# Optimization experiments

Measured on AMD Instinct MI355X. Metric: run time of the kernel, lower is better.

## Reference

```python
import jax, jax.numpy as jnp
import numpy as np

N_NODES = 50000
N_EDGES = 800000
IN_FEAT = 128
OUT_FEAT = 128


def _glorot(key, shape):
    fan_in, fan_out = shape[1], shape[0]
    lim = jnp.sqrt(6.0 / (fan_in + fan_out))
    return jax.random.uniform(key, shape, jnp.float32, -lim, lim)


def setup_inputs() -> dict:
    key = jax.random.key(0)
    ks = jax.random.split(key, 9)
    x = jax.random.normal(ks[0], (N_NODES, IN_FEAT), jnp.float32)
    edge_index = jax.random.randint(ks[1], (2, N_EDGES), 0, N_NODES, jnp.int64)
    # SAGEConv params: lin_l applied to aggregated neighbors (with bias),
    # lin_r applied to root features (no bias) -- PyG default mean aggregation.
    W1l = _glorot(ks[2], (OUT_FEAT, IN_FEAT)); b1l = jnp.zeros((OUT_FEAT,), jnp.float32)
    W1r = _glorot(ks[3], (OUT_FEAT, IN_FEAT))
    W2l = _glorot(ks[4], (OUT_FEAT, OUT_FEAT)); b2l = jnp.zeros((OUT_FEAT,), jnp.float32)
    W2r = _glorot(ks[5], (OUT_FEAT, OUT_FEAT))
    Wlin = _glorot(ks[6], (2, OUT_FEAT)); blin = jnp.zeros((2,), jnp.float32)
    return {"x": x, "edge_index": edge_index,
            "W1l": W1l, "b1l": b1l, "W1r": W1r,
            "W2l": W2l, "b2l": b2l, "W2r": W2r,
            "Wlin": Wlin, "blin": blin}


def _sage_conv(x, src, dst, Wl, bl, Wr, n_nodes):
    # mean-aggregate neighbor features at destination nodes
    agg_sum = jax.ops.segment_sum(x[src], dst, num_segments=n_nodes)  # [N, F]
    deg = jax.ops.segment_sum(jnp.ones((src.shape[0],), x.dtype), dst, num_segments=n_nodes)
    agg = agg_sum / jnp.maximum(deg, 1.0)[:, None]
    return agg @ Wl.T + bl + x @ Wr.T


def reference(x, edge_index, W1l, b1l, W1r, W2l, b2l, W2r, Wlin, blin):
    src, dst = edge_index[0], edge_index[1]
    n = x.shape[0]
    h = _sage_conv(x, src, dst, W1l, b1l, W1r, n)
    h = jax.nn.relu(h)  # dropout is identity in eval mode
    h = _sage_conv(h, src, dst, W2l, b2l, W2r, n)
    h = jax.nn.relu(h)
    logits = h @ Wlin.T + blin  # [N, 2]
    return jax.nn.log_softmax(logits, axis=1)
```

## Files before the change

### kernel.cpp

```cpp
#include <hip/hip_runtime.h>
#include <math.h>

#define N_NODES 50000
#define N_EDGES 800000
#define F 128
#define ELL_CAP 64
#define NBUCK 196
#define BIN_CAP 97
#define BUCK_CAP 4608
#define EDGE_BLKS 125
#define EPR (N_EDGES / EDGE_BLKS)
#define CVT_BLKS 6250

typedef __attribute__((ext_vector_type(8))) short short8;
typedef __attribute__((ext_vector_type(4))) float float4v;

__device__ inline unsigned short f2bf(float f) {
    unsigned int u = __builtin_bit_cast(unsigned int, f);
    u += 0x7FFF + ((u >> 16) & 1);
    return (unsigned short)(u >> 16);
}
__device__ inline float bf2f_lo(unsigned int u) {
    return __builtin_bit_cast(float, u << 16);
}
__device__ inline float bf2f_hi(unsigned int u) {
    return __builtin_bit_cast(float, u & 0xFFFF0000u);
}
__device__ inline float i8f(unsigned int u, int k) {
    return (float)((signed char)(u >> (k * 8)));
}

__global__ __launch_bounds__(256) void prep1(const float* __restrict__ x,
                                             const int* __restrict__ src,
                                             const int* __restrict__ dst,
                                             const float* __restrict__ W1l,
                                             const float* __restrict__ W1r,
                                             const float* __restrict__ W2l,
                                             const float* __restrict__ W2r,
                                             unsigned short* __restrict__ xb,
                                             unsigned char* __restrict__ xq,
                                             float* __restrict__ xscale,
                                             int* __restrict__ tails,
                                             unsigned int* __restrict__ bucketEdges,
                                             unsigned short* __restrict__ P1,
                                             unsigned short* __restrict__ P2) {
    int blk = blockIdx.x;
    int tid = threadIdx.x;
    if (blk < EDGE_BLKS) {
        __shared__ int bin_cnt[NBUCK];
        __shared__ unsigned int bins[NBUCK * BIN_CAP];
        for (int i = tid; i < NBUCK; i += 256) bin_cnt[i] = 0;
        __syncthreads();
        int base = blk * EPR;
        for (int i = tid; i < EPR; i += 256) {
            int d = dst[base + i];
            int s = src[base + i];
            int lb = d >> 8;
            int pos = atomicAdd(&bin_cnt[lb], 1);
            if (pos < BIN_CAP)
                bins[lb * BIN_CAP + pos] = ((unsigned int)(d & 255) << 16) | (unsigned int)s;
        }
        __syncthreads();
        if (tid < NBUCK) {
            int c = bin_cnt[tid]; if (c > BIN_CAP) c = BIN_CAP;
            int rb = atomicAdd(&tails[tid], c);
            unsigned int* dp = bucketEdges + (size_t)tid * BUCK_CAP;
            for (int i = 0; i < c; ++i) {
                int p = rb + i;
                if (p < BUCK_CAP) dp[p] = bins[tid * BIN_CAP + i];
            }
        }
    } else if (blk < EDGE_BLKS + CVT_BLKS) {
        int row = (blk - EDGE_BLKS) * 8 + (tid >> 5);
        int hl = tid & 31;
        float4 v = ((const float4*)x)[row * 32 + hl];
        float m = fmaxf(fmaxf(fabsf(v.x), fabsf(v.y)), fmaxf(fabsf(v.z), fabsf(v.w)));
        #pragma unroll
        for (int off = 1; off < 32; off <<= 1) m = fmaxf(m, __shfl_xor(m, off));
        float inv = m > 0.f ? 127.f / m : 0.f;
        int q0 = (int)rintf(v.x * inv), q1 = (int)rintf(v.y * inv);
        int q2 = (int)rintf(v.z * inv), q3 = (int)rintf(v.w * inv);
        unsigned int qp = (q0 & 255) | ((q1 & 255) << 8) | ((q2 & 255) << 16) | ((q3 & 255) << 24);
        ((unsigned int*)xq)[row * 32 + hl] = qp;
        unsigned int p0 = (unsigned int)f2bf(v.x) | ((unsigned int)f2bf(v.y) << 16);
        unsigned int p1 = (unsigned int)f2bf(v.z) | ((unsigned int)f2bf(v.w) << 16);
        ((uint2*)xb)[row * 32 + hl] = make_uint2(p0, p1);
        if (hl == 0) xscale[row] = m * (1.f / 127.f);
    } else {
        int pblk = blk - (EDGE_BLKS + CVT_BLKS);
        int t = (pblk & 15) * 256 + tid;
        int lane = t & 63;
        int ct = (t >> 6) & 7;
        int ks = t >> 9;
        const float* Wl = (pblk < 16) ? W1l : W2l;
        const float* Wr = (pblk < 16) ? W1r : W2r;
        unsigned short* P = (pblk < 16) ? P1 : P2;
        int col = ct * 16 + (lane & 15);
        int kbase = (ks & 3) * 32 + (lane >> 4) * 8;
        const float* W = (ks < 4) ? Wl : Wr;
        unsigned short* dp = P + (size_t)t * 8;
        #pragma unroll
        for (int j = 0; j < 8; ++j) dp[j] = f2bf(W[col * F + kbase + j]);
    }
}

__global__ __launch_bounds__(256) void ell_build(const int* __restrict__ tails,
                                                 const unsigned int* __restrict__ bucketEdges,
                                                 int* __restrict__ cnt,
                                                 unsigned short* __restrict__ nbr) {
    __shared__ int cl[256];
    __shared__ unsigned short ell[256 * ELL_CAP];
    int b = blockIdx.x;
    int tid = threadIdx.x;
    cl[tid] = 0;
    __syncthreads();
    int T = tails[b]; if (T > BUCK_CAP) T = BUCK_CAP;
    const unsigned int* eb = bucketEdges + (size_t)b * BUCK_CAP;
    for (int i = tid; i < T; i += 256) {
        unsigned int rec = eb[i];
        int nib = rec >> 16;
        int pos = atomicAdd(&cl[nib], 1);
        if (pos < ELL_CAP) ell[nib * ELL_CAP + pos] = (unsigned short)(rec & 0xFFFFu);
    }
    __syncthreads();
    int nb0 = b * 256;
    int nn = N_NODES - nb0; if (nn > 256) nn = 256;
    if (tid < nn) cnt[nb0 + tid] = cl[tid];
    const uint4* s4 = (const uint4*)ell;
    uint4* d4 = (uint4*)(nbr + (size_t)nb0 * ELL_CAP);
    int n4 = nn * (ELL_CAP * 2 / 16);
    for (int i = tid; i < n4; i += 256) d4[i] = s4[i];
}

__global__ __launch_bounds__(256) void aggregate_q(const unsigned char* __restrict__ Xq,
                                                   const float* __restrict__ xs,
                                                   const int* __restrict__ cnt,
                                                   const unsigned short* __restrict__ nbr,
                                                   unsigned short* __restrict__ agg) {
    int tid = threadIdx.x;
    int wave = tid >> 6;
    int lane = tid & 63;
    int half = lane >> 5;
    int hl = lane & 31;
    int node = blockIdx.x * 8 + wave * 2 + half;

    int degt = cnt[node];
    int deg = degt < ELL_CAP ? degt : ELL_CAP;
    const unsigned short* nb = nbr + node * ELL_CAP;
    const unsigned int* Xu = (const unsigned int*)Xq;

    float a0 = 0.f, a1 = 0.f, a2 = 0.f, a3 = 0.f;
    int s = 0;
    for (; s + 4 <= deg; s += 4) {
        ushort4 nv = *(const ushort4*)(nb + s);
        unsigned int g0 = Xu[nv.x * 32 + hl]; float s0 = xs[nv.x];
        unsigned int g1 = Xu[nv.y * 32 + hl]; float s1 = xs[nv.y];
        unsigned int g2 = Xu[nv.z * 32 + hl]; float s2 = xs[nv.z];
        unsigned int g3 = Xu[nv.w * 32 + hl]; float s3 = xs[nv.w];
        a0 += i8f(g0, 0) * s0 + i8f(g1, 0) * s1 + i8f(g2, 0) * s2 + i8f(g3, 0) * s3;
        a1 += i8f(g0, 1) * s0 + i8f(g1, 1) * s1 + i8f(g2, 1) * s2 + i8f(g3, 1) * s3;
        a2 += i8f(g0, 2) * s0 + i8f(g1, 2) * s1 + i8f(g2, 2) * s2 + i8f(g3, 2) * s3;
        a3 += i8f(g0, 3) * s0 + i8f(g1, 3) * s1 + i8f(g2, 3) * s2 + i8f(g3, 3) * s3;
    }
    for (; s < deg; ++s) {
        int v = nb[s];
        unsigned int g = Xu[v * 32 + hl]; float sc = xs[v];
        a0 += i8f(g, 0) * sc; a1 += i8f(g, 1) * sc;
        a2 += i8f(g, 2) * sc; a3 += i8f(g, 3) * sc;
    }
    float inv = 1.0f / (float)(degt > 0 ? degt : 1);
    unsigned int p0 = (unsigned int)f2bf(a0 * inv) | ((unsigned int)f2bf(a1 * inv) << 16);
    unsigned int p1 = (unsigned int)f2bf(a2 * inv) | ((unsigned int)f2bf(a3 * inv) << 16);
    *(uint2*)(agg + (size_t)node * F + hl * 4) = make_uint2(p0, p1);
}

__global__ __launch_bounds__(256) void sage_gemm(const unsigned short* __restrict__ Abf,
                                                 const unsigned short* __restrict__ Bbf,
                                                 const unsigned short* __restrict__ Pw,
                                                 const float* __restrict__ bias,
                                                 unsigned short* __restrict__ Hout,
                                                 unsigned char* __restrict__ Hq,
                                                 float* __restrict__ Hscale,
                                                 const float* __restrict__ Wlin,
                                                 const float* __restrict__ blin,
                                                 float* __restrict__ out, int mode) {
    int lane = threadIdx.x & 63;
    int wave = threadIdx.x >> 6;
    int r0 = blockIdx.x * 64 + wave * 16;
    int rowA = r0 + (lane & 15);
    if (rowA >= N_NODES) rowA = N_NODES - 1;
    int kg = lane >> 4;

    short8 af[4], bfr[4];
    const short8* Ap = (const short8*)(Abf + (size_t)rowA * F);
    const short8* Bp = (const short8*)(Bbf + (size_t)rowA * F);
    #pragma unroll
    for (int ks = 0; ks < 4; ++ks) {
        af[ks]  = Ap[ks * 4 + kg];
        bfr[ks] = Bp[ks * 4 + kg];
    }

    const short8* Wp = (const short8*)Pw;
    float4v acc[8];
    #pragma unroll
    for (int ct = 0; ct < 8; ++ct) {
        float4v c = {0.f, 0.f, 0.f, 0.f};
        #pragma unroll
        for (int ks = 0; ks < 4; ++ks)
            c = __builtin_amdgcn_mfma_f32_16x16x32_bf16(af[ks], Wp[(ks * 8 + ct) * 64 + lane], c, 0, 0, 0);
        #pragma unroll
        for (int ks = 0; ks < 4; ++ks)
            c = __builtin_amdgcn_mfma_f32_16x16x32_bf16(bfr[ks], Wp[((ks + 4) * 8 + ct) * 64 + lane], c, 0, 0, 0);
        acc[ct] = c;
    }

    int colb = lane & 15;
    int rq = lane >> 4;
    #pragma unroll
    for (int ct = 0; ct < 8; ++ct) {
        float bv = bias[ct * 16 + colb];
        #pragma unroll
        for (int i = 0; i < 4; ++i)
            acc[ct][i] = fmaxf(acc[ct][i] + bv, 0.f);
    }

    if (mode == 0) {
        #pragma unroll
        for (int ct = 0; ct < 8; ++ct) {
            #pragma unroll
            for (int i = 0; i < 4; ++i) {
                int row = r0 + rq * 4 + i;
                if (row < N_NODES)
                    Hout[(size_t)row * F + ct * 16 + colb] = f2bf(acc[ct][i]);
            }
        }
        #pragma unroll
        for (int i = 0; i < 4; ++i) {
            float m = 0.f;
            #pragma unroll
            for (int ct = 0; ct < 8; ++ct) m = fmaxf(m, acc[ct][i]);
            #pragma unroll
            for (int off = 1; off < 16; off <<= 1) m = fmaxf(m, __shfl_xor(m, off));
            float inv = m > 0.f ? 127.f / m : 0.f;
            int row = r0 + rq * 4 + i;
            if (row < N_NODES) {
                if (colb == 0) Hscale[row] = m * (1.f / 127.f);
                #pragma unroll
                for (int ct = 0; ct < 8; ++ct) {
                    int q = (int)rintf(acc[ct][i] * inv);
                    Hq[(size_t)row * F + ct * 16 + colb] = (unsigned char)q;
                }
            }
        }
    } else {
        float w0[8], w1[8];
        #pragma unroll
        for (int ct = 0; ct < 8; ++ct) {
            w0[ct] = Wlin[ct * 16 + colb];
            w1[ct] = Wlin[F + ct * 16 + colb];
        }
        #pragma unroll
        for (int i = 0; i < 4; ++i) {
            float p0 = 0.f, p1 = 0.f;
            #pragma unroll
            for (int ct = 0; ct < 8; ++ct) {
                p0 += acc[ct][i] * w0[ct];
                p1 += acc[ct][i] * w1[ct];
            }
            #pragma unroll
            for (int off = 1; off < 16; off <<= 1) {
                p0 += __shfl_xor(p0, off);
                p1 += __shfl_xor(p1, off);
            }
            int row = r0 + rq * 4 + i;
            if (colb == 0 && row < N_NODES) {
                float a = p0 + blin[0];
                float b = p1 + blin[1];
                float m = fmaxf(a, b);
                float lse = m + logf(expf(a - m) + expf(b - m));
                out[(size_t)row * 2 + 0] = a - lse;
                out[(size_t)row * 2 + 1] = b - lse;
            }
        }
    }
}

extern "C" void kernel_launch(void* const* d_in, const int* in_sizes, int n_in,
                              void* d_out, int out_size, void* d_ws, size_t ws_size,
                              hipStream_t stream) {
    const float* x    = (const float*)d_in[0];
    const int*   ei   = (const int*)d_in[1];
    const float* W1l  = (const float*)d_in[2];
    const float* b1l  = (const float*)d_in[3];
    const float* W1r  = (const float*)d_in[4];
    const float* W2l  = (const float*)d_in[5];
    const float* b2l  = (const float*)d_in[6];
    const float* W2r  = (const float*)d_in[7];
    const float* Wlin = (const float*)d_in[8];
    const float* blin = (const float*)d_in[9];
    float* out = (float*)d_out;

    const int* src = ei;
    const int* dst = ei + N_EDGES;

    char* ws = (char*)d_ws;
    int*            tails  = (int*)ws;
    unsigned int*   bEdge  = (unsigned int*)(ws + 4096);
    int*            cnt    = (int*)(ws + 3620864);
    unsigned short* nbr    = (unsigned short*)(ws + 3821568);
    unsigned short* xb     = (unsigned short*)(ws + 10221568);
    unsigned short* h1b    = (unsigned short*)(ws + 23021568);
    unsigned short* aggb   = (unsigned short*)(ws + 35821568);
    unsigned short* P1     = (unsigned short*)(ws + 48621568);
    unsigned short* P2     = (unsigned short*)(ws + 48687104);
    unsigned char*  xq     = (unsigned char*)(ws + 48752640);
    unsigned char*  h1q    = (unsigned char*)(ws + 55152640);
    float*          xscale = (float*)(ws + 61552640);
    float*          h1scale= (float*)(ws + 61752640);

    hipMemsetAsync(tails, 0, NBUCK * sizeof(int), stream);

    prep1<<<EDGE_BLKS + CVT_BLKS + 32, 256, 0, stream>>>(x, src, dst, W1l, W1r, W2l, W2r,
                                                         xb, xq, xscale, tails, bEdge, P1, P2);
    ell_build<<<NBUCK, 256, 0, stream>>>(tails, bEdge, cnt, nbr);

    aggregate_q<<<6250, 256, 0, stream>>>(xq, xscale, cnt, nbr, aggb);
    sage_gemm<<<782, 256, 0, stream>>>(aggb, xb, P1, b1l, h1b, h1q, h1scale,
                                       nullptr, nullptr, nullptr, 0);

    aggregate_q<<<6250, 256, 0, stream>>>(h1q, h1scale, cnt, nbr, aggb);
    sage_gemm<<<782, 256, 0, stream>>>(aggb, h1b, P2, b2l, nullptr, nullptr, nullptr,
                                       Wlin, blin, out, 1);
}
```

Before: 122.1 us.

## Fuse neighbor aggregation into SAGE GEMM via LDS and drop bf16 copies

Merges the aggregation kernel into the GEMM kernel. Each 64-row block gathers int8 neighbor features into a padded LDS tile as bf16, then runs the MFMA GEMM reading A from LDS. The bf16 copies of x and h1 are removed, and the root operand is dequantized from int8 on the fly. This cuts two launches and the global round trip of the aggregate and bf16 feature buffers. In exchange, each block now has fewer waves doing the gather (782 blocks instead of 6250), which may reduce latency hiding, and the root term loses precision from int8 input.

```diff
diff --git a/kernel.cpp b/kernel.cpp
--- a/kernel.cpp
+++ b/kernel.cpp
@@ -11,6 +11,7 @@
 #define EDGE_BLKS 125
 #define EPR (N_EDGES / EDGE_BLKS)
 #define CVT_BLKS 6250
+#define LROW 136
 
 typedef __attribute__((ext_vector_type(8))) short short8;
 typedef __attribute__((ext_vector_type(4))) float float4v;
@@ -20,14 +21,16 @@
     u += 0x7FFF + ((u >> 16) & 1);
     return (unsigned short)(u >> 16);
 }
-__device__ inline float bf2f_lo(unsigned int u) {
-    return __builtin_bit_cast(float, u << 16);
-}
-__device__ inline float bf2f_hi(unsigned int u) {
-    return __builtin_bit_cast(float, u & 0xFFFF0000u);
-}
 __device__ inline float i8f(unsigned int u, int k) {
     return (float)((signed char)(u >> (k * 8)));
+}
+__device__ inline short8 deq8(uint2 g, float sc) {
+    short8 r;
+    #pragma unroll
+    for (int j = 0; j < 4; ++j) r[j] = (short)f2bf(i8f(g.x, j) * sc);
+    #pragma unroll
+    for (int j = 0; j < 4; ++j) r[4 + j] = (short)f2bf(i8f(g.y, j) * sc);
+    return r;
 }
 
 __global__ __launch_bounds__(256) void prep1(const float* __restrict__ x,
@@ -37,7 +40,6 @@
                                              const float* __restrict__ W1r,
                                              const float* __restrict__ W2l,
                                              const float* __restrict__ W2r,
-                                             unsigned short* __restrict__ xb,
                                              unsigned char* __restrict__ xq,
                                              float* __restrict__ xscale,
                                              int* __restrict__ tails,
@@ -82,9 +84,6 @@
         int q2 = (int)rintf(v.z * inv), q3 = (int)rintf(v.w * inv);
         unsigned int qp = (q0 & 255) | ((q1 & 255) << 8) | ((q2 & 255) << 16) | ((q3 & 255) << 24);
         ((unsigned int*)xq)[row * 32 + hl] = qp;
-        unsigned int p0 = (unsigned int)f2bf(v.x) | ((unsigned int)f2bf(v.y) << 16);
-        unsigned int p1 = (unsigned int)f2bf(v.z) | ((unsigned int)f2bf(v.w) << 16);
-        ((uint2*)xb)[row * 32 + hl] = make_uint2(p0, p1);
         if (hl == 0) xscale[row] = m * (1.f / 127.f);
     } else {
         int pblk = blk - (EDGE_BLKS + CVT_BLKS);
@@ -132,72 +131,82 @@
     for (int i = tid; i < n4; i += 256) d4[i] = s4[i];
 }
 
-__global__ __launch_bounds__(256) void aggregate_q(const unsigned char* __restrict__ Xq,
-                                                   const float* __restrict__ xs,
-                                                   const int* __restrict__ cnt,
-                                                   const unsigned short* __restrict__ nbr,
-                                                   unsigned short* __restrict__ agg) {
+__global__ __launch_bounds__(256) void sage_fused(const unsigned char* __restrict__ Xq,
+                                                  const float* __restrict__ xs,
+                                                  const int* __restrict__ cnt,
+                                                  const unsigned short* __restrict__ nbr,
+                                                  const unsigned short* __restrict__ Pw,
+                                                  const float* __restrict__ bias,
+                                                  unsigned char* __restrict__ Hq,
+                                                  float* __restrict__ Hscale,
+                                                  const float* __restrict__ Wlin,
+                                                  const float* __restrict__ blin,
+                                                  float* __restrict__ out, int mode) {
+    __shared__ unsigned short sA[64 * LROW];
     int tid = threadIdx.x;
     int wave = tid >> 6;
     int lane = tid & 63;
-    int half = lane >> 5;
-    int hl = lane & 31;
-    int node = blockIdx.x * 8 + wave * 2 + half;
-
-    int degt = cnt[node];
-    int deg = degt < ELL_CAP ? degt : ELL_CAP;
-    const unsigned short* nb = nbr + node * ELL_CAP;
-    const unsigned int* Xu = (const unsigned int*)Xq;
-
-    float a0 = 0.f, a1 = 0.f, a2 = 0.f, a3 = 0.f;
-    int s = 0;
-    for (; s + 4 <= deg; s += 4) {
-        ushort4 nv = *(const ushort4*)(nb + s);
-        unsigned int g0 = Xu[nv.x * 32 + hl]; float s0 = xs[nv.x];
-        unsigned int g1 = Xu[nv.y * 32 + hl]; float s1 = xs[nv.y];
-        unsigned int g2 = Xu[nv.z * 32 + hl]; float s2 = xs[nv.z];
-        unsigned int g3 = Xu[nv.w * 32 + hl]; float s3 = xs[nv.w];
-        a0 += i8f(g0, 0) * s0 + i8f(g1, 0) * s1 + i8f(g2, 0) * s2 + i8f(g3, 0) * s3;
-        a1 += i8f(g0, 1) * s0 + i8f(g1, 1) * s1 + i8f(g2, 1) * s2 + i8f(g3, 1) * s3;
-        a2 += i8f(g0, 2) * s0 + i8f(g1, 2) * s1 + i8f(g2, 2) * s2 + i8f(g3, 2) * s3;
-        a3 += i8f(g0, 3) * s0 + i8f(g1, 3) * s1 + i8f(g2, 3) * s2 + i8f(g3, 3) * s3;
-    }
-    for (; s < deg; ++s) {
-        int v = nb[s];
-        unsigned int g = Xu[v * 32 + hl]; float sc = xs[v];
-        a0 += i8f(g, 0) * sc; a1 += i8f(g, 1) * sc;
-        a2 += i8f(g, 2) * sc; a3 += i8f(g, 3) * sc;
-    }
-    float inv = 1.0f / (float)(degt > 0 ? degt : 1);
-    unsigned int p0 = (unsigned int)f2bf(a0 * inv) | ((unsigned int)f2bf(a1 * inv) << 16);
-    unsigned int p1 = (unsigned int)f2bf(a2 * inv) | ((unsigned int)f2bf(a3 * inv) << 16);
-    *(uint2*)(agg + (size_t)node * F + hl * 4) = make_uint2(p0, p1);
-}
-
-__global__ __launch_bounds__(256) void sage_gemm(const unsigned short* __restrict__ Abf,
-                                                 const unsigned short* __restrict__ Bbf,
-                                                 const unsigned short* __restrict__ Pw,
-                                                 const float* __restrict__ bias,
-                                                 unsigned short* __restrict__ Hout,
-                                                 unsigned char* __restrict__ Hq,
-                                                 float* __restrict__ Hscale,
-                                                 const float* __restrict__ Wlin,
-                                                 const float* __restrict__ blin,
-                                                 float* __restrict__ out, int mode) {
-    int lane = threadIdx.x & 63;
-    int wave = threadIdx.x >> 6;
-    int r0 = blockIdx.x * 64 + wave * 16;
-    int rowA = r0 + (lane & 15);
-    if (rowA >= N_NODES) rowA = N_NODES - 1;
+    int nb0 = blockIdx.x * 64;
+
+    int q = lane >> 4;
+    int ql = lane & 15;
+    const uint2* Xu2 = (const uint2*)Xq;
+    #pragma unroll
+    for (int round = 0; round < 4; ++round) {
+        int r = wave * 16 + round * 4 + q;
+        int node = nb0 + r;
+        float a0 = 0.f, a1 = 0.f, a2 = 0.f, a3 = 0.f, a4 = 0.f, a5 = 0.f, a6 = 0.f, a7 = 0.f;
+        int degt = 0;
+        if (node < N_NODES) {
+            degt = cnt[node];
+            int deg = degt < ELL_CAP ? degt : ELL_CAP;
+            const unsigned short* nb = nbr + node * ELL_CAP;
+            int s = 0;
+            for (; s + 4 <= deg; s += 4) {
+                ushort4 nv = *(const ushort4*)(nb + s);
+                uint2 g0 = Xu2[nv.x * 16 + ql]; float s0 = xs[nv.x];
+                uint2 g1 = Xu2[nv.y * 16 + ql]; float s1 = xs[nv.y];
+                uint2 g2 = Xu2[nv.z * 16 + ql]; float s2 = xs[nv.z];
+                uint2 g3 = Xu2[nv.w * 16 + ql]; float s3 = xs[nv.w];
+                a0 += i8f(g0.x, 0) * s0 + i8f(g1.x, 0) * s1 + i8f(g2.x, 0) * s2 + i8f(g3.x, 0) * s3;
+                a1 += i8f(g0.x, 1) * s0 + i8f(g1.x, 1) * s1 + i8f(g2.x, 1) * s2 + i8f(g3.x, 1) * s3;
+                a2 += i8f(g0.x, 2) * s0 + i8f(g1.x, 2) * s1 + i8f(g2.x, 2) * s2 + i8f(g3.x, 2) * s3;
+                a3 += i8f(g0.x, 3) * s0 + i8f(g1.x, 3) * s1 + i8f(g2.x, 3) * s2 + i8f(g3.x, 3) * s3;
+                a4 += i8f(g0.y, 0) * s0 + i8f(g1.y, 0) * s1 + i8f(g2.y, 0) * s2 + i8f(g3.y, 0) * s3;
+                a5 += i8f(g0.y, 1) * s0 + i8f(g1.y, 1) * s1 + i8f(g2.y, 1) * s2 + i8f(g3.y, 1) * s3;
+                a6 += i8f(g0.y, 2) * s0 + i8f(g1.y, 2) * s1 + i8f(g2.y, 2) * s2 + i8f(g3.y, 2) * s3;
+                a7 += i8f(g0.y, 3) * s0 + i8f(g1.y, 3) * s1 + i8f(g2.y, 3) * s2 + i8f(g3.y, 3) * s3;
+            }
+            for (; s < deg; ++s) {
+                int v = nb[s];
+                uint2 g = Xu2[v * 16 + ql]; float sc = xs[v];
+                a0 += i8f(g.x, 0) * sc; a1 += i8f(g.x, 1) * sc;
+                a2 += i8f(g.x, 2) * sc; a3 += i8f(g.x, 3) * sc;
+                a4 += i8f(g.y, 0) * sc; a5 += i8f(g.y, 1) * sc;
+                a6 += i8f(g.y, 2) * sc; a7 += i8f(g.y, 3) * sc;
+            }
+        }
+        float inv = 1.0f / (float)(degt > 0 ? degt : 1);
+        unsigned int w0 = (unsigned int)f2bf(a0 * inv) | ((unsigned int)f2bf(a1 * inv) << 16);
+        unsigned int w1 = (unsigned int)f2bf(a2 * inv) | ((unsigned int)f2bf(a3 * inv) << 16);
+        unsigned int w2 = (unsigned int)f2bf(a4 * inv) | ((unsigned int)f2bf(a5 * inv) << 16);
+        unsigned int w3 = (unsigned int)f2bf(a6 * inv) | ((unsigned int)f2bf(a7 * inv) << 16);
+        *(uint4*)(sA + r * LROW + ql * 8) = make_uint4(w0, w1, w2, w3);
+    }
+    __syncthreads();
+
+    int lrow = wave * 16 + (lane & 15);
+    int rowB = nb0 + lrow; if (rowB >= N_NODES) rowB = N_NODES - 1;
     int kg = lane >> 4;
 
     short8 af[4], bfr[4];
-    const short8* Ap = (const short8*)(Abf + (size_t)rowA * F);
-    const short8* Bp = (const short8*)(Bbf + (size_t)rowA * F);
+    const short8* Ash = (const short8*)sA;
+    const uint2* Bu = (const uint2*)(Xq + (size_t)rowB * F);
+    float bs = xs[rowB];
     #pragma unroll
     for (int ks = 0; ks < 4; ++ks) {
-        af[ks]  = Ap[ks * 4 + kg];
-        bfr[ks] = Bp[ks * 4 + kg];
+        af[ks]  = Ash[lrow * 17 + ks * 4 + kg];
+        bfr[ks] = deq8(Bu[ks * 4 + kg], bs);
     }
 
     const short8* Wp = (const short8*)Pw;
@@ -216,6 +225,7 @@
 
     int colb = lane & 15;
     int rq = lane >> 4;
+    int r0 = nb0 + wave * 16;
     #pragma unroll
     for (int ct = 0; ct < 8; ++ct) {
         float bv = bias[ct * 16 + colb];
@@ -225,15 +235,6 @@
     }
 
     if (mode == 0) {
-        #pragma unroll
-        for (int ct = 0; ct < 8; ++ct) {
-            #pragma unroll
-            for (int i = 0; i < 4; ++i) {
-                int row = r0 + rq * 4 + i;
-                if (row < N_NODES)
-                    Hout[(size_t)row * F + ct * 16 + colb] = f2bf(acc[ct][i]);
-            }
-        }
         #pragma unroll
         for (int i = 0; i < 4; ++i) {
             float m = 0.f;
@@ -247,8 +248,8 @@
                 if (colb == 0) Hscale[row] = m * (1.f / 127.f);
                 #pragma unroll
                 for (int ct = 0; ct < 8; ++ct) {
-                    int q = (int)rintf(acc[ct][i] * inv);
-                    Hq[(size_t)row * F + ct * 16 + colb] = (unsigned char)q;
+                    int qv = (int)rintf(acc[ct][i] * inv);
+                    Hq[(size_t)row * F + ct * 16 + colb] = (unsigned char)qv;
                 }
             }
         }
@@ -308,27 +309,22 @@
     unsigned int*   bEdge  = (unsigned int*)(ws + 4096);
     int*            cnt    = (int*)(ws + 3620864);
     unsigned short* nbr    = (unsigned short*)(ws + 3821568);
-    unsigned short* xb     = (unsigned short*)(ws + 10221568);
-    unsigned short* h1b    = (unsigned short*)(ws + 23021568);
-    unsigned short* aggb   = (unsigned short*)(ws + 35821568);
-    unsigned short* P1     = (unsigned short*)(ws + 48621568);
-    unsigned short* P2     = (unsigned short*)(ws + 48687104);
-    unsigned char*  xq     = (unsigned char*)(ws + 48752640);
-    unsigned char*  h1q    = (unsigned char*)(ws + 55152640);
-    float*          xscale = (float*)(ws + 61552640);
-    float*          h1scale= (float*)(ws + 61752640);
+    unsigned char*  xq     = (unsigned char*)(ws + 10221568);
+    unsigned char*  h1q    = (unsigned char*)(ws + 16621568);
+    float*          xscale = (float*)(ws + 23021568);
+    float*          h1scale= (float*)(ws + 23221568);
+    unsigned short* P1     = (unsigned short*)(ws + 23421568);
+    unsigned short* P2     = (unsigned short*)(ws + 23487104);
 
     hipMemsetAsync(tails, 0, NBUCK * sizeof(int), stream);
 
     prep1<<<EDGE_BLKS + CVT_BLKS + 32, 256, 0, stream>>>(x, src, dst, W1l, W1r, W2l, W2r,
-                                                         xb, xq, xscale, tails, bEdge, P1, P2);
+                                                         xq, xscale, tails, bEdge, P1, P2);
     ell_build<<<NBUCK, 256, 0, stream>>>(tails, bEdge, cnt, nbr);
 
-    aggregate_q<<<6250, 256, 0, stream>>>(xq, xscale, cnt, nbr, aggb);
-    sage_gemm<<<782, 256, 0, stream>>>(aggb, xb, P1, b1l, h1b, h1q, h1scale,
-                                       nullptr, nullptr, nullptr, 0);
-
-    aggregate_q<<<6250, 256, 0, stream>>>(h1q, h1scale, cnt, nbr, aggb);
-    sage_gemm<<<782, 256, 0, stream>>>(aggb, h1b, P2, b2l, nullptr, nullptr, nullptr,
-                                       Wlin, blin, out, 1);
-}
+    sage_fused<<<782, 256, 0, stream>>>(xq, xscale, cnt, nbr, P1, b1l, h1q, h1scale,
+                                        nullptr, nullptr, nullptr, 0);
+
+    sage_fused<<<782, 256, 0, stream>>>(h1q, h1scale, cnt, nbr, P2, b2l, nullptr, nullptr,
+                                        Wlin, blin, out, 1);
+}
```

Result: slower. 155.7 us (+27.5%).
